# Performance work log

Hardware: AMD Instinct MI355X
Metric: run time of the kernel (lower is better)

The kernel has to match this reference:

```python
import jax, jax.numpy as jnp
import numpy as np

N = 50000      # nodes
E = 800000     # edges per relation
R = 3          # relations
FEAT = 64      # feat_len
HID = 64       # h_dim
NUM_PRED = 5
S = 8192       # seeds


def setup_inputs() -> dict:
    key = jax.random.key(0)
    ks = jax.random.split(key, 24)
    p = lambda k, s: jax.random.normal(k, s, jnp.float32) * 0.05
    x = jax.random.normal(ks[0], (N, FEAT), jnp.float32)
    noise = jax.random.normal(ks[1], (N, HID), jnp.float32)
    seeds = jax.random.randint(ks[2], (S,), 0, N)
    edges = [jax.random.randint(ks[3 + i], (E,), 0, N) for i in range(2 * R)]
    return dict(
        x=x, noise=noise, seeds=seeds,
        src0=edges[0], dst0=edges[1], src1=edges[2], dst1=edges[3],
        src2=edges[4], dst2=edges[5],
        W_conv1=p(ks[9], (R, FEAT, HID)), b_conv1=jnp.zeros((HID,), jnp.float32),
        W_conv2=p(ks[10], (R, HID, HID)), b_conv2=jnp.zeros((HID,), jnp.float32),
        W_lin=p(ks[11], (HID, HID)), b_lin=jnp.zeros((HID,), jnp.float32),
        dW1=p(ks[12], (R, HID, 256)), db1=jnp.zeros((R, 256), jnp.float32),
        dW2=p(ks[13], (R, 256, 32)), db2=jnp.zeros((R, 32), jnp.float32),
        dW3=p(ks[14], (R, 32, 1)), db3=jnp.zeros((R, 1), jnp.float32),
        fW1=p(ks[15], (R, HID, 256)), fb1=jnp.zeros((R, 256), jnp.float32),
        fW2=p(ks[16], (R, 256, 2048)), fb2=jnp.zeros((R, 2048), jnp.float32),
        fW3=p(ks[17], (R, 2048, FEAT * NUM_PRED)), fb3=jnp.zeros((R, FEAT * NUM_PRED), jnp.float32),
    )


def _rel_conv(h, srcs, dsts, W, b):
    # DGL RelGraphConvLayer: per-relation GraphConv(norm='right'), summed over
    # relations (HeteroGraphConv aggregate='sum'), + bias, ReLU (dropout=0).
    out_dim = W.shape[2]
    acc = jnp.zeros((N, out_dim), h.dtype)
    for r in range(R):
        m = (h @ W[r])[srcs[r]]                                   # [E, out]
        agg = jnp.zeros((N, out_dim), h.dtype).at[dsts[r]].add(m)
        deg = jnp.zeros((N,), h.dtype).at[dsts[r]].add(1.0)
        acc = acc + agg / jnp.maximum(deg, 1.0)[:, None]          # norm='right'
    return jax.nn.relu(acc + b)


def reference(x, noise, W_conv1, b_conv1, W_conv2, b_conv2, W_lin, b_lin,
              dW1, db1, dW2, db2, dW3, db3,
              fW1, fb1, fW2, fb2, fW3, fb3,
              seeds, src0, dst0, src1, dst1, src2, dst2):
    srcs = (src0, src1, src2)
    dsts = (dst0, dst1, dst2)
    # two stacked relational conv layers
    h = _rel_conv(x, srcs, dsts, W_conv1, b_conv1)
    h = _rel_conv(h, srcs, dsts, W_conv2, b_conv2)
    # per-ntype Linear + LeakyReLU (dropout=0)
    h = jax.nn.leaky_relu(h @ W_lin + b_lin)
    # Sampler: additive Gaussian noise
    h = h + noise
    # dGen/fGen index inputs[ntype][ind] with ind = enumerate position -> first S rows
    hs = h[:seeds.shape[0]]                                       # [S, HID]
    # ReldGen: per-relation MLP HID->256->32->1 (LeakyReLU, final ReLU)
    z = jax.nn.leaky_relu(jnp.einsum('sd,rdh->rsh', hs, dW1) + db1[:, None, :])
    z = jax.nn.leaky_relu(jnp.einsum('rsh,rhk->rsk', z, dW2) + db2[:, None, :])
    pred_missing = jax.nn.relu(jnp.einsum('rsk,rko->rso', z, dW3) + db3[:, None, :])  # [R,S,1]
    # RelfGen: per-relation MLP HID->256->2048->FEAT*NUM_PRED (ReLU, final Tanh)
    z = jax.nn.relu(jnp.einsum('sd,rdh->rsh', hs, fW1) + fb1[:, None, :])
    z = jax.nn.relu(jnp.einsum('rsh,rhk->rsk', z, fW2) + fb2[:, None, :])
    pred_feat = jnp.tanh(jnp.einsum('rsk,rko->rso', z, fW3) + fb3[:, None, :])        # [R,S,NUM_PRED*FEAT]
    # pack (pred_missing, pred_feat) into one array [R, S, 1 + NUM_PRED*FEAT]
    return jnp.concatenate([pred_missing, pred_feat], axis=-1)
```

## Files before the change

kernel.cpp:

```cpp
#include <hip/hip_runtime.h>
#include <math.h>

#define N_NODES 50000
#define N_EDGES 800000
#define RELS    3
#define HID     64
#define S_SEEDS 8192
#define OUT_COLS 321
#define S_CH    4096
#define NB      391
#define BCAP    2560
#define CHUNK   4096
#define NCHUNK  196

typedef __attribute__((ext_vector_type(8))) _Float16 v8h;
typedef __attribute__((ext_vector_type(4))) float v4f;
typedef __attribute__((ext_vector_type(2))) _Float16 h2;

__device__ __forceinline__ unsigned short f32_to_f16(float f) {
    _Float16 h = (_Float16)f;
    return __builtin_bit_cast(unsigned short, h);
}
__device__ __forceinline__ float f16_to_f32(unsigned short u) {
    return (float)__builtin_bit_cast(_Float16, u);
}
__device__ __forceinline__ h2 u2h2(unsigned u) { return __builtin_bit_cast(h2, u); }
__device__ __forceinline__ unsigned h2u(h2 h) { return __builtin_bit_cast(unsigned, h); }

template<int ACT, bool OUT_F16, int BN, int BM = 128>
__global__ __launch_bounds__(256) void gemm_mfma_f16(
    const unsigned short* __restrict__ A, long long sAb, int lda,
    const unsigned short* __restrict__ Bt, long long sBb,
    const float* __restrict__ bias, long long sBiasb,
    void* __restrict__ Cv, long long sCb, int ldc,
    const float* __restrict__ noise,
    int M, int Nc, int K)
{
    constexpr int WC = (BN == 128 || BM == 64) ? 2 : 1;
    constexpr int WR = 4 / WC;
    constexpr int TI = BM / (WR * 16);
    constexpr int TJ = BN / (WC * 16);
    constexpr int TPRA = 256 / BM;
    constexpr int TPRB = 256 / BN;

    __shared__ __align__(16) unsigned short As[2][BM][40];
    __shared__ __align__(16) unsigned short Bs[2][BN][40];

    const int r = blockIdx.z;
    A  += (long long)r * sAb;
    Bt += (long long)r * sBb;
    const float* brow = bias ? bias + (long long)r * sBiasb : nullptr;

    int bx = blockIdx.x, by = blockIdx.y;
    {
        const int nwg  = gridDim.x * gridDim.y;
        const int orig = by * gridDim.x + bx;
        const int q = nwg >> 3, rm = nwg & 7;
        const int xcd = orig & 7, idx = orig >> 3;
        const int wg = (xcd < rm ? xcd * (q + 1) : rm * (q + 1) + (xcd - rm) * q) + idx;
        bx = wg % gridDim.x;
        by = wg / gridDim.x;
    }

    const int tid  = threadIdx.x;
    const int wave = tid >> 6, lane = tid & 63;
    const int quad = lane >> 4, l16 = lane & 15;
    const int wrow = (wave / WC) * (TI * 16);
    const int wcol = (wave % WC) * (TJ * 16);
    const int row0 = by * BM, col0 = bx * BN;

    v4f acc[TI][TJ] = {};

    const int srow = tid / TPRA;
    const int ecol = (tid % TPRA) * (32 / TPRA);
    const int brw  = tid / TPRB;
    const int bcl  = (tid % TPRB) * (32 / TPRB);

    const int gr = row0 + srow;
    const bool aval = (gr < M);
    const unsigned short* aptr = A + (long long)gr * lda + ecol;
    const int gn = col0 + brw;
    const bool bval = (gn < Nc);
    const unsigned short* bptr = Bt + (long long)gn * K + bcl;

    struct Tile { int4 a0, a1, b0, b1; };
    auto loadT = [&](Tile& t, int k0) {
        t.a0 = make_int4(0, 0, 0, 0); t.a1 = make_int4(0, 0, 0, 0);
        t.b0 = make_int4(0, 0, 0, 0); t.b1 = make_int4(0, 0, 0, 0);
        if (aval) {
            t.a0 = *(const int4*)(aptr + k0);
            if constexpr (TPRA == 2) t.a1 = *(const int4*)(aptr + k0 + 8);
        }
        if (bval) {
            t.b0 = *(const int4*)(bptr + k0);
            if constexpr (TPRB == 2) t.b1 = *(const int4*)(bptr + k0 + 8);
        }
    };
    auto storeT = [&](const Tile& t, int buf) {
        *(int4*)(&As[buf][srow][ecol]) = t.a0;
        if constexpr (TPRA == 2) *(int4*)(&As[buf][srow][ecol + 8]) = t.a1;
        *(int4*)(&Bs[buf][brw][bcl]) = t.b0;
        if constexpr (TPRB == 2) *(int4*)(&Bs[buf][brw][bcl + 8]) = t.b1;
    };
    auto compute = [&](int buf) {
        v8h af[TI], bfr[TJ];
#pragma unroll
        for (int i = 0; i < TI; i++)
            af[i] = *(const v8h*)(&As[buf][wrow + i * 16 + l16][quad * 8]);
#pragma unroll
        for (int j = 0; j < TJ; j++)
            bfr[j] = *(const v8h*)(&Bs[buf][wcol + j * 16 + l16][quad * 8]);
#pragma unroll
        for (int i = 0; i < TI; i++)
#pragma unroll
            for (int j = 0; j < TJ; j++)
                acc[i][j] = __builtin_amdgcn_mfma_f32_16x16x32_f16(af[i], bfr[j], acc[i][j], 0, 0, 0);
    };

    const int nt = K >> 5;

    Tile tX, tY;
    loadT(tX, 0);
    storeT(tX, 0);
    if (nt > 1) loadT(tX, 32);
    __syncthreads();

    int cur = 0;
    int t = 0;
    for (; t + 2 < nt; t += 2) {
        loadT(tY, (t + 2) * 32);
        compute(cur);
        storeT(tX, cur ^ 1);
        __syncthreads();
        cur ^= 1;
        if (t + 3 < nt) loadT(tX, (t + 3) * 32);
        compute(cur);
        storeT(tY, cur ^ 1);
        __syncthreads();
        cur ^= 1;
    }
    if (t + 1 < nt) {
        compute(cur);
        storeT(tX, cur ^ 1);
        __syncthreads();
        cur ^= 1;
    }
    compute(cur);

    float* Cf = (float*)Cv + (long long)r * sCb;
    unsigned short* Ch = (unsigned short*)Cv + (long long)r * sCb;
#pragma unroll
    for (int i = 0; i < TI; i++) {
#pragma unroll
        for (int j = 0; j < TJ; j++) {
            int gc = col0 + wcol + j * 16 + l16;
            if (gc >= Nc) continue;
            float bv = brow ? brow[gc] : 0.f;
#pragma unroll
            for (int tt = 0; tt < 4; tt++) {
                int grr = row0 + wrow + i * 16 + quad * 4 + tt;
                if (grr >= M) continue;
                float v = acc[i][j][tt] + bv;
                if (ACT == 1)      v = fmaxf(v, 0.f);
                else if (ACT == 2) v = (v > 0.f) ? v : 0.01f * v;
                else if (ACT == 3) v = tanhf(v);
                if (noise) v += noise[(long long)grr * ldc + gc];
                if (OUT_F16) Ch[(long long)grr * ldc + gc] = f32_to_f16(v);
                else         Cf[(long long)grr * ldc + gc] = v;
            }
        }
    }
}

__global__ void cvt_f32_f16_kernel(const float* __restrict__ src,
                                   unsigned short* __restrict__ dst, long long n)
{
    long long i = (long long)blockIdx.x * blockDim.x + threadIdx.x;
    if (i < n) dst[i] = f32_to_f16(src[i]);
}

struct TD { const float* s; unsigned short* d; int K, N, nbx, nby, b0; };
struct TDs { TD v[8]; };

__global__ __launch_bounds__(256) void transpose_all_kernel(TDs ds)
{
    __shared__ float t[32][33];
    int b = blockIdx.x;
    int k = 0;
#pragma unroll
    for (int q = 1; q < 8; q++) if (b >= ds.v[q].b0) k = q;
    TD td = ds.v[k];
    int local = b - td.b0;
    int per_r = td.nbx * td.nby;
    int r  = local / per_r;
    int rem = local - r * per_r;
    int by = rem / td.nbx, bx = rem - by * td.nbx;

    const float* src = td.s + (long long)r * td.K * td.N;
    unsigned short* dst = td.d + (long long)r * td.K * td.N;
    int n0 = bx * 32, k0 = by * 32;
    int tx = threadIdx.x & 31, ty = threadIdx.x >> 5;
#pragma unroll
    for (int i = 0; i < 32; i += 8) {
        int kk = k0 + ty + i, n = n0 + tx;
        if (kk < td.K && n < td.N) t[ty + i][tx] = src[(long long)kk * td.N + n];
    }
    __syncthreads();
#pragma unroll
    for (int i = 0; i < 32; i += 8) {
        int n = n0 + ty + i, kk = k0 + tx;
        if (n < td.N && kk < td.K) dst[(long long)n * td.K + kk] = f32_to_f16(t[tx][ty + i]);
    }
}

__global__ __launch_bounds__(256) void bin_fill_kernel(
    const int* __restrict__ s0, const int* __restrict__ d0,
    const int* __restrict__ s1, const int* __restrict__ d1,
    const int* __restrict__ s2, const int* __restrict__ d2,
    int* __restrict__ gcursor,
    unsigned int* __restrict__ bedges)
{
    __shared__ int cnt[NB];
    __shared__ int lstart[NB];
    __shared__ int fillc[NB];
    __shared__ int gstart[NB];
    __shared__ int scan[512];
    __shared__ unsigned int svals[CHUNK];
    __shared__ short sbuck[CHUNK];

    const int rel = blockIdx.y;
    const int* sp = (rel == 0) ? s0 : (rel == 1) ? s1 : s2;
    const int* dp = (rel == 0) ? d0 : (rel == 1) ? d1 : d2;
    const int tid = threadIdx.x;
    const int e0 = blockIdx.x * CHUNK;
    const int n  = min(CHUNK, N_EDGES - e0);

    for (int i = tid; i < NB; i += 256) { cnt[i] = 0; fillc[i] = 0; }
    __syncthreads();

    int myb[CHUNK / 256];
    unsigned int myv[CHUNK / 256];
#pragma unroll
    for (int i = 0; i < CHUNK / 256; i++) {
        int off = tid + i * 256;
        if (off < n) {
            int e = e0 + off;
            int s = sp[e], d = dp[e];
            int b = d >> 7;
            myb[i] = b;
            myv[i] = ((unsigned int)(d & 127) << 16) | (unsigned int)s;
            atomicAdd(&cnt[b], 1);
        } else myb[i] = -1;
    }
    __syncthreads();

    scan[tid]       = (tid < NB) ? cnt[tid] : 0;
    scan[tid + 256] = (tid + 256 < NB) ? cnt[tid + 256] : 0;
    __syncthreads();
    for (int off = 1; off < 512; off <<= 1) {
        int a = (tid >= off) ? scan[tid - off] : 0;
        int b = (tid + 256 >= off) ? scan[tid + 256 - off] : 0;
        __syncthreads();
        scan[tid] += a; scan[tid + 256] += b;
        __syncthreads();
    }
    if (tid < NB)       lstart[tid]       = scan[tid] - cnt[tid];
    if (tid + 256 < NB) lstart[tid + 256] = scan[tid + 256] - cnt[tid + 256];
    __syncthreads();

#pragma unroll
    for (int i = 0; i < CHUNK / 256; i++) {
        int b = myb[i];
        if (b >= 0) {
            int p = lstart[b] + atomicAdd(&fillc[b], 1);
            svals[p] = myv[i];
            sbuck[p] = (short)b;
        }
    }
    if (tid < NB && cnt[tid] > 0)
        gstart[tid] = atomicAdd(&gcursor[rel * NB + tid], cnt[tid]);
    if (tid + 256 < NB && cnt[tid + 256] > 0)
        gstart[tid + 256] = atomicAdd(&gcursor[rel * NB + tid + 256], cnt[tid + 256]);
    __syncthreads();

    for (int p = tid; p < n; p += 256) {
        int b = sbuck[p];
        int pos = gstart[b] + (p - lstart[b]);
        bedges[(long long)(rel * NB + b) * BCAP + pos] = svals[p];
    }
}

__global__ __launch_bounds__(256) void bucket_csr_kernel(
    const unsigned int* __restrict__ bedges,
    const int* __restrict__ gcursor,
    unsigned short* __restrict__ csr16,
    int* __restrict__ browptr)
{
    __shared__ int cnt[128], sc[128], start[128], cur[128];
    __shared__ unsigned short ssorted[BCAP];

    const int id  = blockIdx.y * NB + blockIdx.x;
    const int tid = threadIdx.x;
    const int len = gcursor[id];
    const unsigned int* ep = bedges + (long long)id * BCAP;

    for (int i = tid; i < 128; i += 256) cnt[i] = 0;
    __syncthreads();
    for (int i = tid; i < len; i += 256)
        atomicAdd(&cnt[ep[i] >> 16], 1);
    __syncthreads();

    int v = (tid < 128) ? cnt[tid] : 0;
    if (tid < 128) sc[tid] = v;
    __syncthreads();
    for (int off = 1; off < 128; off <<= 1) {
        int a = (tid < 128 && tid >= off) ? sc[tid - off] : 0;
        __syncthreads();
        if (tid < 128) sc[tid] += a;
        __syncthreads();
    }
    if (tid < 128) { start[tid] = sc[tid] - v; cur[tid] = sc[tid] - v; }
    __syncthreads();

    for (int i = tid; i < len; i += 256) {
        unsigned int vv = ep[i];
        int dl = vv >> 16;
        int pos = atomicAdd(&cur[dl], 1);
        ssorted[pos] = (unsigned short)(vv & 0xFFFFu);
    }
    __syncthreads();

    for (int i = tid; i < len; i += 256)
        csr16[(long long)id * BCAP + i] = ssorted[i];
    if (tid < 128) browptr[id * 128 + tid] = start[tid];
}

__global__ __launch_bounds__(256) void gather_csr_f16_kernel(
    const unsigned short* __restrict__ feat,
    const unsigned short* __restrict__ csr16,
    const int* __restrict__ browptr,
    const int* __restrict__ gcursor,
    unsigned short* __restrict__ agg,
    int M)
{
    int d = (blockIdx.x * 256 + threadIdx.x) >> 6;
    int lane = threadIdx.x & 63;
    if (d >= M) return;
    int bucket = d >> 7, dl = d & 127;
    const int g = lane >> 4;
    const unsigned fo = (unsigned)((lane & 15) << 2);

    int p0[RELS], p1[RELS];
#pragma unroll
    for (int r = 0; r < RELS; r++) {
        int id = r * NB + bucket;
        p0[r] = browptr[id * 128 + dl];
        p1[r] = (dl == 127) ? gcursor[id] : browptr[id * 128 + dl + 1];
    }

    unsigned short* outp = agg + (long long)d * (RELS * HID);

#pragma unroll
    for (int r = 0; r < RELS; r++) {
        const unsigned short* cp = csr16 + (long long)(r * NB + bucket) * BCAP;
        h2 aA01 = (h2)0, aA23 = (h2)0, aB01 = (h2)0, aB23 = (h2)0;
        const int e1 = p1[r];
        int i = p0[r] + g;
        for (; i + 12 < e1; i += 16) {
            unsigned s0 = cp[i], s1 = cp[i + 4], s2 = cp[i + 8], s3 = cp[i + 12];
            uint2 w0 = *(const uint2*)(feat + (s0 << 6) + fo);
            uint2 w1 = *(const uint2*)(feat + (s1 << 6) + fo);
            uint2 w2 = *(const uint2*)(feat + (s2 << 6) + fo);
            uint2 w3 = *(const uint2*)(feat + (s3 << 6) + fo);
            aA01 += u2h2(w0.x) + u2h2(w1.x);
            aA23 += u2h2(w0.y) + u2h2(w1.y);
            aB01 += u2h2(w2.x) + u2h2(w3.x);
            aB23 += u2h2(w2.y) + u2h2(w3.y);
        }
        if (i + 4 < e1) {
            unsigned s0 = cp[i], s1 = cp[i + 4];
            uint2 w0 = *(const uint2*)(feat + (s0 << 6) + fo);
            uint2 w1 = *(const uint2*)(feat + (s1 << 6) + fo);
            aA01 += u2h2(w0.x) + u2h2(w1.x);
            aA23 += u2h2(w0.y) + u2h2(w1.y);
            i += 8;
        }
        if (i < e1) {
            unsigned s0 = cp[i];
            uint2 w0 = *(const uint2*)(feat + (s0 << 6) + fo);
            aB01 += u2h2(w0.x);
            aB23 += u2h2(w0.y);
        }
        h2 a01 = aA01 + aB01, a23 = aA23 + aB23;

        a01 += u2h2((unsigned)__shfl_xor((int)h2u(a01), 16));
        a23 += u2h2((unsigned)__shfl_xor((int)h2u(a23), 16));
        a01 += u2h2((unsigned)__shfl_xor((int)h2u(a01), 32));
        a23 += u2h2((unsigned)__shfl_xor((int)h2u(a23), 32));

        if (lane < 16) {
            float inv = 1.0f / fmaxf((float)(e1 - p0[r]), 1.0f);
            ushort4 o;
            o.x = f32_to_f16((float)a01.x * inv);
            o.y = f32_to_f16((float)a01.y * inv);
            o.z = f32_to_f16((float)a23.x * inv);
            o.w = f32_to_f16((float)a23.y * inv);
            *(ushort4*)(outp + r * HID + fo) = o;
        }
    }
}

__global__ void dhead_kernel(const float* __restrict__ z2d,
                             const float* __restrict__ dW3,
                             const float* __restrict__ db3,
                             float* __restrict__ out)
{
    int idx = blockIdx.x * blockDim.x + threadIdx.x;
    if (idx >= RELS * S_SEEDS) return;
    int r = idx / S_SEEDS;
    const float* zp = z2d + (long long)idx * 32;
    const float* wp = dW3 + r * 32;
    float acc = db3[r];
#pragma unroll
    for (int k = 0; k < 32; k++) acc += zp[k] * wp[k];
    out[(long long)idx * OUT_COLS] = fmaxf(acc, 0.f);
}

extern "C" void kernel_launch(void* const* d_in, const int* in_sizes, int n_in,
                              void* d_out, int out_size, void* d_ws, size_t ws_size,
                              hipStream_t stream)
{
    const float* x     = (const float*)d_in[0];
    const float* noise = (const float*)d_in[1];
    const int* srcs[RELS] = { (const int*)d_in[3], (const int*)d_in[5], (const int*)d_in[7] };
    const int* dsts[RELS] = { (const int*)d_in[4], (const int*)d_in[6], (const int*)d_in[8] };
    const float* Wc1  = (const float*)d_in[9];
    const float* bc1  = (const float*)d_in[10];
    const float* Wc2  = (const float*)d_in[11];
    const float* bc2  = (const float*)d_in[12];
    const float* Wlin = (const float*)d_in[13];
    const float* blin = (const float*)d_in[14];
    const float* dW1  = (const float*)d_in[15];
    const float* db1  = (const float*)d_in[16];
    const float* dW2  = (const float*)d_in[17];
    const float* db2  = (const float*)d_in[18];
    const float* dW3  = (const float*)d_in[19];
    const float* db3  = (const float*)d_in[20];
    const float* fW1  = (const float*)d_in[21];
    const float* fb1  = (const float*)d_in[22];
    const float* fW2  = (const float*)d_in[23];
    const float* fb2  = (const float*)d_in[24];
    const float* fW3  = (const float*)d_in[25];
    const float* fb3  = (const float*)d_in[26];
    float* out = (float*)d_out;
    float* w   = (float*)d_ws;

    int* gcursor = (int*)w;
    int* browptr = (int*)(w + 1280);
    unsigned short* csr16 = (unsigned short*)(w + 151424);
    unsigned short* aggx_hf = (unsigned short*)(w + 1652864);
    unsigned int*   bedges  = (unsigned int*)(w + 1652864 + 2400000);
    float*          z2d     = w + 1652864 + 2400000;
    unsigned short* z2hf    = (unsigned short*)(w + 1652864);
    unsigned short* xhf  = (unsigned short*)(w + 14235776);
    unsigned short* z1hf = (unsigned short*)(w + 14235776);
    unsigned short* h1hf   = (unsigned short*)(w + 17381504);
    unsigned short* agg2hf = (unsigned short*)(w + 18981504);
    unsigned short* h2shf  = (unsigned short*)(w + 19767936);
    unsigned short* hshf   = (unsigned short*)(w + 20030080);
    unsigned short* WcT1   = (unsigned short*)(w + 20292224);
    unsigned short* WcT2   = (unsigned short*)(w + 20298368);
    unsigned short* WlinT  = (unsigned short*)(w + 20304512);
    unsigned short* dW1ht  = (unsigned short*)(w + 20306560);
    unsigned short* dW2ht  = (unsigned short*)(w + 20331136);
    unsigned short* fW1ht  = (unsigned short*)(w + 20343424);
    unsigned short* fW2ht  = (unsigned short*)(w + 20368000);
    unsigned short* fW3ht  = (unsigned short*)(w + 21154432);

    hipMemsetAsync(gcursor, 0, (size_t)RELS * NB * sizeof(int), stream);
    bin_fill_kernel<<<dim3(NCHUNK, RELS), 256, 0, stream>>>(
        srcs[0], dsts[0], srcs[1], dsts[1], srcs[2], dsts[2], gcursor, bedges);
    bucket_csr_kernel<<<dim3(NB, RELS), 256, 0, stream>>>(
        bedges, gcursor, csr16, browptr);

    cvt_f32_f16_kernel<<<(N_NODES * HID + 255) / 256, 256, 0, stream>>>(x, xhf, (long long)N_NODES * HID);
    {
        TDs ds;
        int b0 = 0;
        auto add = [&](int k, const float* s, unsigned short* d, int K, int N, int rels) {
            ds.v[k].s = s; ds.v[k].d = d; ds.v[k].K = K; ds.v[k].N = N;
            ds.v[k].nbx = (N + 31) / 32; ds.v[k].nby = (K + 31) / 32; ds.v[k].b0 = b0;
            b0 += ds.v[k].nbx * ds.v[k].nby * rels;
        };
        add(0, Wc1, WcT1, 192, 64, 1);
        add(1, Wc2, WcT2, 192, 64, 1);
        add(2, Wlin, WlinT, 64, 64, 1);
        add(3, dW1, dW1ht, 64, 256, RELS);
        add(4, dW2, dW2ht, 256, 32, RELS);
        add(5, fW1, fW1ht, 64, 256, RELS);
        add(6, fW2, fW2ht, 256, 2048, RELS);
        add(7, fW3, fW3ht, 2048, 320, RELS);
        transpose_all_kernel<<<b0, 256, 0, stream>>>(ds);
    }

    gather_csr_f16_kernel<<<(N_NODES + 3) / 4, 256, 0, stream>>>(
        xhf, csr16, browptr, gcursor, aggx_hf, N_NODES);
    gemm_mfma_f16<1, true, 64, 64><<<dim3(1, (N_NODES + 63) / 64, 1), 256, 0, stream>>>(
        aggx_hf, 0, RELS * HID, WcT1, 0, bc1, 0,
        h1hf, 0, HID, nullptr, N_NODES, HID, RELS * HID);

    gather_csr_f16_kernel<<<(S_SEEDS + 3) / 4, 256, 0, stream>>>(
        h1hf, csr16, browptr, gcursor, agg2hf, S_SEEDS);
    gemm_mfma_f16<1, true, 64, 64><<<dim3(1, S_SEEDS / 64, 1), 256, 0, stream>>>(
        agg2hf, 0, RELS * HID, WcT2, 0, bc2, 0,
        h2shf, 0, HID, nullptr, S_SEEDS, HID, RELS * HID);

    gemm_mfma_f16<2, true, 64, 64><<<dim3(1, S_SEEDS / 64, 1), 256, 0, stream>>>(
        h2shf, 0, HID, WlinT, 0, blin, 0,
        hshf, 0, HID, noise, S_SEEDS, HID, HID);

    gemm_mfma_f16<2, true, 128><<<dim3(2, S_SEEDS / 128, RELS), 256, 0, stream>>>(
        hshf, 0, HID, dW1ht, 256LL * 64, db1, 256,
        z1hf, (long long)S_SEEDS * 256, 256, nullptr, S_SEEDS, 256, HID);
    gemm_mfma_f16<2, false, 64, 64><<<dim3(1, S_SEEDS / 64, RELS), 256, 0, stream>>>(
        z1hf, (long long)S_SEEDS * 256, 256, dW2ht, 32LL * 256, db2, 32,
        z2d, (long long)S_SEEDS * 32, 32, nullptr, S_SEEDS, 32, 256);
    dhead_kernel<<<(RELS * S_SEEDS + 255) / 256, 256, 0, stream>>>(z2d, dW3, db3, out);

    gemm_mfma_f16<1, true, 128><<<dim3(2, S_SEEDS / 128, RELS), 256, 0, stream>>>(
        hshf, 0, HID, fW1ht, 256LL * 64, fb1, 256,
        z1hf, (long long)S_SEEDS * 256, 256, nullptr, S_SEEDS, 256, HID);
    for (int c = 0; c < S_SEEDS / S_CH; c++) {
        long long s0 = (long long)c * S_CH;
        gemm_mfma_f16<1, true, 128><<<dim3(2048 / 128, S_CH / 128, RELS), 256, 0, stream>>>(
            z1hf + s0 * 256, (long long)S_SEEDS * 256, 256,
            fW2ht, 2048LL * 256, fb2, 2048,
            z2hf, (long long)S_CH * 2048, 2048, nullptr, S_CH, 2048, 256);
        gemm_mfma_f16<3, false, 64, 64><<<dim3(5, S_CH / 64, RELS), 256, 0, stream>>>(
            z2hf, (long long)S_CH * 2048, 2048,
            fW3ht, 320LL * 2048, fb3, 320,
            out + s0 * OUT_COLS + 1, (long long)S_SEEDS * OUT_COLS, OUT_COLS,
            nullptr, S_CH, 320, 2048);
    }
}
```

Measured before the change: 492.0 us.

## Fuse fGen second and third layers into one kernel keeping hidden tile on-chip

Replaces the chunked pair of GEMM launches (256->2048 with ReLU, then 2048->320 with tanh) with a single kernel. Each block takes 128 seeds of one relation and walks the 2048-wide hidden dimension in 64-column slices, computing each slice into shared memory and immediately accumulating it into the 320-wide output. This removes the write and re-read of the large fp16 intermediate in global memory and two launches per chunk. In exchange it uses a large shared-memory footprint and holds many accumulators per thread, and only 192 blocks are launched, which may limit occupancy and parallelism.

```diff
diff --git a/kernel.cpp b/kernel.cpp
--- a/kernel.cpp
+++ b/kernel.cpp
@@ -7,7 +7,6 @@
 #define HID     64
 #define S_SEEDS 8192
 #define OUT_COLS 321
-#define S_CH    4096
 #define NB      391
 #define BCAP    2560
 #define CHUNK   4096
@@ -170,6 +169,166 @@
             }
         }
     }
+}
+
+__global__ __launch_bounds__(512) void fused_f23_kernel(
+    const unsigned short* __restrict__ z1,
+    const unsigned short* __restrict__ fW2t,
+    const float* __restrict__ fb2,
+    const unsigned short* __restrict__ fW3t,
+    const float* __restrict__ fb3,
+    float* __restrict__ out)
+{
+    __shared__ __align__(16) unsigned short Bs2[64 * 256];
+    __shared__ __align__(16) unsigned short Bs3[320 * 64];
+    __shared__ __align__(16) unsigned short Z2[128 * 64];
+    __shared__ float Fb2[2048];
+
+    int orig = blockIdx.y * gridDim.x + blockIdx.x;
+    {
+        const int q = (gridDim.x * gridDim.y) >> 3;
+        orig = (orig & 7) * q + (orig >> 3);
+    }
+    const int rel = orig / gridDim.x;
+    const int s0  = (orig % gridDim.x) * 128;
+
+    const int tid = threadIdx.x;
+    const int wave = tid >> 6;
+    const int lane = tid & 63;
+    const int quad = lane >> 4, l16 = lane & 15;
+    const int wr = wave >> 1;
+    const int wc = wave & 1;
+
+    const unsigned short* z1p = z1 + ((long long)rel * S_SEEDS + s0) * 256;
+    const unsigned short* w2p = fW2t + (long long)rel * 2048 * 256;
+    const unsigned short* w3p = fW3t + (long long)rel * 320 * 2048;
+
+    for (int u = tid; u < 2048; u += 512) Fb2[u] = fb2[rel * 2048 + u];
+
+    v8h zfr[2][8];
+#pragma unroll
+    for (int i = 0; i < 2; i++) {
+        const unsigned short* rp = z1p + (wr * 32 + i * 16 + l16) * 256 + quad * 8;
+#pragma unroll
+        for (int ks = 0; ks < 8; ks++)
+            zfr[i][ks] = *(const v8h*)(rp + ks * 32);
+    }
+
+    int4 sr2[4], sr3[5];
+    auto stageLoad = [&](int h0) {
+#pragma unroll
+        for (int u = 0; u < 4; u++) {
+            int g = tid + u * 512;
+            int row = g >> 5, gc = g & 31;
+            sr2[u] = *(const int4*)(w2p + (h0 + row) * 256 + gc * 8);
+        }
+#pragma unroll
+        for (int u = 0; u < 5; u++) {
+            int g = tid + u * 512;
+            int n = g >> 3, gc = g & 7;
+            sr3[u] = *(const int4*)(w3p + (long long)n * 2048 + h0 + gc * 8);
+        }
+    };
+    auto stageWrite = [&]() {
+        char* b2 = (char*)Bs2; char* b3 = (char*)Bs3;
+#pragma unroll
+        for (int u = 0; u < 4; u++) {
+            int g = tid + u * 512;
+            int row = g >> 5, gc = g & 31;
+            *(int4*)(b2 + row * 512 + ((gc * 16) ^ ((row & 7) << 4))) = sr2[u];
+        }
+#pragma unroll
+        for (int u = 0; u < 5; u++) {
+            int g = tid + u * 512;
+            int n = g >> 3, gc = g & 7;
+            *(int4*)(b3 + n * 128 + ((gc * 16) ^ ((n & 7) << 4))) = sr3[u];
+        }
+    };
+
+    v4f acc3[2][10] = {};
+
+    stageLoad(0);
+    stageWrite();
+    __syncthreads();
+
+    for (int c = 0; c < 32; c++) {
+        const int h0 = c * 64;
+        v4f a2[2][2] = {};
+        const char* cb2 = (const char*)Bs2;
+#pragma unroll
+        for (int ks = 0; ks < 8; ks++) {
+            v8h bf[2];
+#pragma unroll
+            for (int j = 0; j < 2; j++) {
+                int hl = wc * 32 + j * 16 + l16;
+                bf[j] = *(const v8h*)(cb2 + hl * 512 +
+                        ((ks * 64 + quad * 16) ^ ((hl & 7) << 4)));
+            }
+#pragma unroll
+            for (int i = 0; i < 2; i++)
+#pragma unroll
+                for (int j = 0; j < 2; j++)
+                    a2[i][j] = __builtin_amdgcn_mfma_f32_16x16x32_f16(zfr[i][ks], bf[j], a2[i][j], 0, 0, 0);
+        }
+        if (c + 1 < 32) stageLoad(h0 + 64);
+        char* zb = (char*)Z2;
+#pragma unroll
+        for (int i = 0; i < 2; i++)
+#pragma unroll
+            for (int j = 0; j < 2; j++) {
+                int col = wc * 32 + j * 16 + l16;
+                float bv = Fb2[h0 + col];
+#pragma unroll
+                for (int t = 0; t < 4; t++) {
+                    int row = wr * 32 + i * 16 + quad * 4 + t;
+                    float v = fmaxf(a2[i][j][t] + bv, 0.f);
+                    *(unsigned short*)(zb + row * 128 +
+                        ((col * 2) ^ ((row & 7) << 4))) = f32_to_f16(v);
+                }
+            }
+        __syncthreads();
+#pragma unroll
+        for (int ks = 0; ks < 2; ks++) {
+            v8h af[2], bf3[10];
+#pragma unroll
+            for (int i = 0; i < 2; i++) {
+                int row = wr * 32 + i * 16 + l16;
+                af[i] = *(const v8h*)((const char*)Z2 + row * 128 +
+                        ((ks * 64 + quad * 16) ^ ((row & 7) << 4)));
+            }
+#pragma unroll
+            for (int j = 0; j < 10; j++) {
+                int n = wc * 160 + j * 16 + l16;
+                bf3[j] = *(const v8h*)((const char*)Bs3 + n * 128 +
+                        ((ks * 64 + quad * 16) ^ ((n & 7) << 4)));
+            }
+#pragma unroll
+            for (int i = 0; i < 2; i++)
+#pragma unroll
+                for (int j = 0; j < 10; j++)
+                    acc3[i][j] = __builtin_amdgcn_mfma_f32_16x16x32_f16(af[i], bf3[j], acc3[i][j], 0, 0, 0);
+        }
+        __syncthreads();
+        if (c + 1 < 32) {
+            stageWrite();
+            __syncthreads();
+        }
+    }
+
+    const float* fb3p = fb3 + rel * 320;
+    float* op = out + ((long long)(rel * S_SEEDS + s0)) * OUT_COLS + 1;
+#pragma unroll
+    for (int i = 0; i < 2; i++)
+#pragma unroll
+        for (int j = 0; j < 10; j++) {
+            int col = wc * 160 + j * 16 + l16;
+            float bv = fb3p[col];
+#pragma unroll
+            for (int t = 0; t < 4; t++) {
+                int row = wr * 32 + i * 16 + quad * 4 + t;
+                op[(long long)row * OUT_COLS + col] = tanhf(acc3[i][j][t] + bv);
+            }
+        }
 }
 
 __global__ void cvt_f32_f16_kernel(const float* __restrict__ src,
@@ -461,7 +620,6 @@
     unsigned short* aggx_hf = (unsigned short*)(w + 1652864);
     unsigned int*   bedges  = (unsigned int*)(w + 1652864 + 2400000);
     float*          z2d     = w + 1652864 + 2400000;
-    unsigned short* z2hf    = (unsigned short*)(w + 1652864);
     unsigned short* xhf  = (unsigned short*)(w + 14235776);
     unsigned short* z1hf = (unsigned short*)(w + 14235776);
     unsigned short* h1hf   = (unsigned short*)(w + 17381504);
@@ -530,16 +688,6 @@
     gemm_mfma_f16<1, true, 128><<<dim3(2, S_SEEDS / 128, RELS), 256, 0, stream>>>(
         hshf, 0, HID, fW1ht, 256LL * 64, fb1, 256,
         z1hf, (long long)S_SEEDS * 256, 256, nullptr, S_SEEDS, 256, HID);
-    for (int c = 0; c < S_SEEDS / S_CH; c++) {
-        long long s0 = (long long)c * S_CH;
-        gemm_mfma_f16<1, true, 128><<<dim3(2048 / 128, S_CH / 128, RELS), 256, 0, stream>>>(
-            z1hf + s0 * 256, (long long)S_SEEDS * 256, 256,
-            fW2ht, 2048LL * 256, fb2, 2048,
-            z2hf, (long long)S_CH * 2048, 2048, nullptr, S_CH, 2048, 256);
-        gemm_mfma_f16<3, false, 64, 64><<<dim3(5, S_CH / 64, RELS), 256, 0, stream>>>(
-            z2hf, (long long)S_CH * 2048, 2048,
-            fW3ht, 320LL * 2048, fb3, 320,
-            out + s0 * OUT_COLS + 1, (long long)S_SEEDS * OUT_COLS, OUT_COLS,
-            nullptr, S_CH, 320, 2048);
-    }
-}
+    fused_f23_kernel<<<dim3(S_SEEDS / 128, RELS), 512, 0, stream>>>(
+        z1hf, fW2ht, fb2, fW3ht, fb3, out);
+}
```

Measured after the change: 459.8 us. 1.07x faster.
